# Kernel tuning notes

Measured on AMD Instinct MI355X. Metric: run time of the kernel, lower is better.

The kernel has to match this reference:

```python
import jax, jax.numpy as jnp
import numpy as np

N_NODES = 10000
N_PAIRS = 200000
NUM_FEATURES = 384
DEGREES = [1, 2, 3]
NHEADS = len(DEGREES)
F_HEAD = NUM_FEATURES // NHEADS  # 128
REPEATS = np.array([2 * d + 1 for d in DEGREES])  # [3,5,7]
SPH_DIM = int(REPEATS.sum())  # 15


def setup_inputs() -> dict:
    key = jax.random.key(0)
    ks = jax.random.split(key, 10)
    return {
        "chi": jax.random.normal(ks[0], (N_NODES, SPH_DIM), dtype=jnp.float32),
        "sph_ij": jax.random.normal(ks[1], (N_PAIRS, SPH_DIM), dtype=jnp.float32),
        "x": jax.random.normal(ks[2], (N_NODES, NUM_FEATURES), dtype=jnp.float32),
        "w_ij": jax.random.normal(ks[3], (N_PAIRS, NUM_FEATURES), dtype=jnp.float32),
        "idx_i": jax.random.randint(ks[4], (N_PAIRS,), 0, N_NODES),
        "phi_r_cut": jax.random.uniform(ks[5], (N_PAIRS, 1), dtype=jnp.float32),
        "phi_chi_cut": jax.random.uniform(ks[6], (N_PAIRS,), dtype=jnp.float32),
        "idx_j": jax.random.randint(ks[7], (N_PAIRS,), 0, N_NODES),
        # per-head linear weights (nn.Linear stores (out, in); y = x @ W.T)
        "Wq": jax.random.normal(ks[8], (NHEADS, F_HEAD, F_HEAD), dtype=jnp.float32) / np.sqrt(F_HEAD),
        "Wk": jax.random.normal(ks[9], (NHEADS, F_HEAD, F_HEAD), dtype=jnp.float32) / np.sqrt(F_HEAD),
    }


def reference(chi, sph_ij, x, w_ij, idx_i, phi_r_cut, phi_chi_cut, idx_j, Wq, Wk):
    n = x.shape[0]
    # split into heads: (n, H, Fh) / (E, H, Fh)
    x_h = x.reshape(n, NHEADS, F_HEAD)
    w_h = w_ij.reshape(-1, NHEADS, F_HEAD)
    # per-head linears (vmapped Linear, no bias): y = x @ W.T
    q = jnp.einsum("nhf,hgf->nhg", x_h, Wq)  # (n, H, Fh)
    k = jnp.einsum("nhf,hgf->nhg", x_h, Wk)  # (n, H, Fh)
    # gather + elementwise attention coefficients per head: (E, H)
    alpha = (q[idx_i] * w_h * k[idx_j]).sum(-1) / np.sqrt(F_HEAD).astype(np.float32)
    # combine radial and sphc cutoffs
    alpha = alpha * phi_r_cut + alpha * phi_chi_cut[:, None]  # (E, H)
    # repeat each head over its 2l+1 spherical components -> (E, SPH_DIM)
    alpha_rep = jnp.repeat(alpha, REPEATS, axis=-1, total_repeat_length=SPH_DIM)
    # scatter-add messages into center atoms -> (n, SPH_DIM)
    chi_ = jax.ops.segment_sum(alpha_rep * sph_ij, idx_i, num_segments=n)
    return chi_
```

## Files before the change

### kernel.cpp

```cpp
#include <hip/hip_runtime.h>
#include <hip/hip_bf16.h>

#define N_NODES 10000
#define N_PAIRS 200000
#define NFEAT 384
#define FH 128
#define SPH 15

typedef __bf16 bf16x8 __attribute__((ext_vector_type(8)));
typedef float f32x4 __attribute__((ext_vector_type(4)));

__global__ void cvt4_kernel(const float* __restrict__ in, unsigned short* __restrict__ out, int n4) {
    int t = blockIdx.x * blockDim.x + threadIdx.x;
    if (t >= n4) return;
    float4 v = ((const float4*)in)[t];
    __hip_bfloat16 b0 = __float2bfloat16(v.x);
    __hip_bfloat16 b1 = __float2bfloat16(v.y);
    __hip_bfloat16 b2 = __float2bfloat16(v.z);
    __hip_bfloat16 b3 = __float2bfloat16(v.w);
    ushort4 o;
    o.x = __builtin_bit_cast(unsigned short, b0);
    o.y = __builtin_bit_cast(unsigned short, b1);
    o.z = __builtin_bit_cast(unsigned short, b2);
    o.w = __builtin_bit_cast(unsigned short, b3);
    ((ushort4*)out)[t] = o;
}

__global__ void qk_gemm_kernel(const unsigned short* __restrict__ xb,
                               const unsigned short* __restrict__ Wqb,
                               const unsigned short* __restrict__ Wkb,
                               float* __restrict__ q, float* __restrict__ k) {
    const int head = blockIdx.y;
    const int node0 = blockIdx.x * 16;
    const int wave = threadIdx.x >> 6;
    const int lane = threadIdx.x & 63;
    const int mrow = lane & 15;
    const int quad = lane >> 4;
    const unsigned short* xrow = xb + (size_t)(node0 + mrow) * NFEAT + head * FH + quad * 8;
    for (int task = wave; task < 16; task += 4) {
        const int mat = task & 1;
        const int g0 = (task >> 1) * 16;
        const unsigned short* Wrow =
            (mat ? Wkb : Wqb) + (size_t)head * FH * FH + (size_t)(g0 + mrow) * FH + quad * 8;
        f32x4 acc = {0.f, 0.f, 0.f, 0.f};
#pragma unroll
        for (int k0 = 0; k0 < FH; k0 += 32) {
            bf16x8 a = *(const bf16x8*)(xrow + k0);
            bf16x8 b = *(const bf16x8*)(Wrow + k0);
            acc = __builtin_amdgcn_mfma_f32_16x16x32_bf16(a, b, acc, 0, 0, 0);
        }
        float* dst = mat ? k : q;
        const int g = g0 + (lane & 15);
#pragma unroll
        for (int r = 0; r < 4; ++r) {
            const int node = node0 + quad * 4 + r;
            dst[(size_t)node * NFEAT + head * FH + g] = acc[r];
        }
    }
}

__global__ void pair_kernel(const float* __restrict__ q, const float* __restrict__ kk,
                            const float* __restrict__ w_ij, const float* __restrict__ sph,
                            const int* __restrict__ idx_i, const int* __restrict__ idx_j,
                            const float* __restrict__ phi_r, const float* __restrict__ phi_chi,
                            float* __restrict__ out) {
    const int lane = threadIdx.x & 63;
    const int wid = blockIdx.x * (blockDim.x >> 6) + (threadIdx.x >> 6);
    const int nw = gridDim.x * (blockDim.x >> 6);
    for (int e = wid; e < N_PAIRS; e += nw) {
        const int i = idx_i[e];
        const int j = idx_j[e];
        const float* qr = q + (size_t)i * NFEAT;
        const float* kr = kk + (size_t)j * NFEAT;
        const float* wr = w_ij + (size_t)e * NFEAT;
        float dot[3];
#pragma unroll
        for (int h = 0; h < 3; ++h) {
            const int f = h * FH + 2 * lane;
            float2 q2 = *(const float2*)(qr + f);
            float2 w2 = *(const float2*)(wr + f);
            float2 k2 = *(const float2*)(kr + f);
            float p = q2.x * w2.x * k2.x + q2.y * w2.y * k2.y;
#pragma unroll
            for (int off = 32; off; off >>= 1) p += __shfl_xor(p, off, 64);
            dot[h] = p;
        }
        const float scale = (phi_r[e] + phi_chi[e]) * 0.088388347648318447f;
        if (lane < SPH) {
            const int h = (lane < 3) ? 0 : (lane < 8 ? 1 : 2);
            const float val = dot[h] * scale * sph[(size_t)e * SPH + lane];
            unsafeAtomicAdd(&out[(size_t)i * SPH + lane], val);
        }
    }
}

extern "C" void kernel_launch(void* const* d_in, const int* in_sizes, int n_in,
                              void* d_out, int out_size, void* d_ws, size_t ws_size,
                              hipStream_t stream) {
    const float* sph     = (const float*)d_in[1];
    const float* x       = (const float*)d_in[2];
    const float* w_ij    = (const float*)d_in[3];
    const int*   idx_i   = (const int*)d_in[4];
    const float* phi_r   = (const float*)d_in[5];
    const float* phi_chi = (const float*)d_in[6];
    const int*   idx_j   = (const int*)d_in[7];
    const float* Wq      = (const float*)d_in[8];
    const float* Wk      = (const float*)d_in[9];
    float* out = (float*)d_out;

    char* ws = (char*)d_ws;
    float* qws = (float*)ws;
    float* kws = (float*)(ws + 15360000);
    unsigned short* xb  = (unsigned short*)(ws + 30720000);
    unsigned short* Wqb = (unsigned short*)(ws + 38400000);
    unsigned short* Wkb = (unsigned short*)(ws + 38498304);

    hipMemsetAsync(d_out, 0, (size_t)out_size * sizeof(float), stream);

    cvt4_kernel<<<3750, 256, 0, stream>>>(x, xb, N_NODES * NFEAT / 4);
    cvt4_kernel<<<48, 256, 0, stream>>>(Wq, Wqb, 3 * FH * FH / 4);
    cvt4_kernel<<<48, 256, 0, stream>>>(Wk, Wkb, 3 * FH * FH / 4);

    qk_gemm_kernel<<<dim3(N_NODES / 16, 3), 256, 0, stream>>>(xb, Wqb, Wkb, qws, kws);

    pair_kernel<<<2048, 256, 0, stream>>>(qws, kws, w_ij, sph, idx_i, idx_j,
                                          phi_r, phi_chi, out);
}
```

Baseline: 507.7 us.

## Fuse bf16 conversion into QK GEMM and process four pairs per wave

```diff
diff --git a/kernel.cpp b/kernel.cpp
--- a/kernel.cpp
+++ b/kernel.cpp
@@ -10,25 +10,18 @@
 typedef __bf16 bf16x8 __attribute__((ext_vector_type(8)));
 typedef float f32x4 __attribute__((ext_vector_type(4)));
 
-__global__ void cvt4_kernel(const float* __restrict__ in, unsigned short* __restrict__ out, int n4) {
-    int t = blockIdx.x * blockDim.x + threadIdx.x;
-    if (t >= n4) return;
-    float4 v = ((const float4*)in)[t];
-    __hip_bfloat16 b0 = __float2bfloat16(v.x);
-    __hip_bfloat16 b1 = __float2bfloat16(v.y);
-    __hip_bfloat16 b2 = __float2bfloat16(v.z);
-    __hip_bfloat16 b3 = __float2bfloat16(v.w);
-    ushort4 o;
-    o.x = __builtin_bit_cast(unsigned short, b0);
-    o.y = __builtin_bit_cast(unsigned short, b1);
-    o.z = __builtin_bit_cast(unsigned short, b2);
-    o.w = __builtin_bit_cast(unsigned short, b3);
-    ((ushort4*)out)[t] = o;
+__device__ inline bf16x8 cvt8(const float* __restrict__ p) {
+    float4 lo = *(const float4*)p;
+    float4 hi = *(const float4*)(p + 4);
+    bf16x8 r;
+    r[0] = (__bf16)lo.x; r[1] = (__bf16)lo.y; r[2] = (__bf16)lo.z; r[3] = (__bf16)lo.w;
+    r[4] = (__bf16)hi.x; r[5] = (__bf16)hi.y; r[6] = (__bf16)hi.z; r[7] = (__bf16)hi.w;
+    return r;
 }
 
-__global__ void qk_gemm_kernel(const unsigned short* __restrict__ xb,
-                               const unsigned short* __restrict__ Wqb,
-                               const unsigned short* __restrict__ Wkb,
+__global__ void qk_gemm_kernel(const float* __restrict__ x,
+                               const float* __restrict__ Wq,
+                               const float* __restrict__ Wk,
                                float* __restrict__ q, float* __restrict__ k) {
     const int head = blockIdx.y;
     const int node0 = blockIdx.x * 16;
@@ -36,21 +29,24 @@
     const int lane = threadIdx.x & 63;
     const int mrow = lane & 15;
     const int quad = lane >> 4;
-    const unsigned short* xrow = xb + (size_t)(node0 + mrow) * NFEAT + head * FH + quad * 8;
+    const float* xrow = x + (size_t)(node0 + mrow) * NFEAT + head * FH + quad * 8;
+    bf16x8 afrag[4];
+#pragma unroll
+    for (int t = 0; t < 4; ++t) afrag[t] = cvt8(xrow + t * 32);
+
     for (int task = wave; task < 16; task += 4) {
         const int mat = task & 1;
         const int g0 = (task >> 1) * 16;
-        const unsigned short* Wrow =
-            (mat ? Wkb : Wqb) + (size_t)head * FH * FH + (size_t)(g0 + mrow) * FH + quad * 8;
+        const float* Wrow =
+            (mat ? Wk : Wq) + (size_t)head * FH * FH + (size_t)(g0 + mrow) * FH + quad * 8;
         f32x4 acc = {0.f, 0.f, 0.f, 0.f};
 #pragma unroll
-        for (int k0 = 0; k0 < FH; k0 += 32) {
-            bf16x8 a = *(const bf16x8*)(xrow + k0);
-            bf16x8 b = *(const bf16x8*)(Wrow + k0);
-            acc = __builtin_amdgcn_mfma_f32_16x16x32_bf16(a, b, acc, 0, 0, 0);
+        for (int t = 0; t < 4; ++t) {
+            bf16x8 b = cvt8(Wrow + t * 32);
+            acc = __builtin_amdgcn_mfma_f32_16x16x32_bf16(afrag[t], b, acc, 0, 0, 0);
         }
         float* dst = mat ? k : q;
-        const int g = g0 + (lane & 15);
+        const int g = g0 + mrow;
 #pragma unroll
         for (int r = 0; r < 4; ++r) {
             const int node = node0 + quad * 4 + r;
@@ -65,31 +61,46 @@
                             const float* __restrict__ phi_r, const float* __restrict__ phi_chi,
                             float* __restrict__ out) {
     const int lane = threadIdx.x & 63;
+    const int sub = lane & 15;
+    const int grp = lane >> 4;
     const int wid = blockIdx.x * (blockDim.x >> 6) + (threadIdx.x >> 6);
     const int nw = gridDim.x * (blockDim.x >> 6);
-    for (int e = wid; e < N_PAIRS; e += nw) {
-        const int i = idx_i[e];
-        const int j = idx_j[e];
-        const float* qr = q + (size_t)i * NFEAT;
-        const float* kr = kk + (size_t)j * NFEAT;
-        const float* wr = w_ij + (size_t)e * NFEAT;
-        float dot[3];
+    for (int base = wid * 4; base < N_PAIRS; base += nw * 4) {
+        const int e = base + grp;
+        if (e < N_PAIRS) {
+            const int i = idx_i[e];
+            const int j = idx_j[e];
+            const float* qr = q + (size_t)i * NFEAT;
+            const float* kr = kk + (size_t)j * NFEAT;
+            const float* wr = w_ij + (size_t)e * NFEAT;
+            float dot[3];
 #pragma unroll
-        for (int h = 0; h < 3; ++h) {
-            const int f = h * FH + 2 * lane;
-            float2 q2 = *(const float2*)(qr + f);
-            float2 w2 = *(const float2*)(wr + f);
-            float2 k2 = *(const float2*)(kr + f);
-            float p = q2.x * w2.x * k2.x + q2.y * w2.y * k2.y;
+            for (int h = 0; h < 3; ++h) {
+                const int f = h * FH + sub * 8;
+                float4 qa = *(const float4*)(qr + f);
+                float4 qb = *(const float4*)(qr + f + 4);
+                float4 wa = *(const float4*)(wr + f);
+                float4 wb = *(const float4*)(wr + f + 4);
+                float4 ka = *(const float4*)(kr + f);
+                float4 kb = *(const float4*)(kr + f + 4);
+                float p = qa.x * wa.x * ka.x;
+                p = fmaf(qa.y * wa.y, ka.y, p);
+                p = fmaf(qa.z * wa.z, ka.z, p);
+                p = fmaf(qa.w * wa.w, ka.w, p);
+                p = fmaf(qb.x * wb.x, kb.x, p);
+                p = fmaf(qb.y * wb.y, kb.y, p);
+                p = fmaf(qb.z * wb.z, kb.z, p);
+                p = fmaf(qb.w * wb.w, kb.w, p);
 #pragma unroll
-            for (int off = 32; off; off >>= 1) p += __shfl_xor(p, off, 64);
-            dot[h] = p;
-        }
-        const float scale = (phi_r[e] + phi_chi[e]) * 0.088388347648318447f;
-        if (lane < SPH) {
-            const int h = (lane < 3) ? 0 : (lane < 8 ? 1 : 2);
-            const float val = dot[h] * scale * sph[(size_t)e * SPH + lane];
-            unsafeAtomicAdd(&out[(size_t)i * SPH + lane], val);
+                for (int off = 8; off; off >>= 1) p += __shfl_xor(p, off, 16);
+                dot[h] = p;
+            }
+            const float scale = (phi_r[e] + phi_chi[e]) * 0.088388347648318447f;
+            if (sub < SPH) {
+                const int h = (sub < 3) ? 0 : (sub < 8 ? 1 : 2);
+                const float val = dot[h] * scale * sph[(size_t)e * SPH + sub];
+                unsafeAtomicAdd(&out[(size_t)i * SPH + sub], val);
+            }
         }
     }
 }
@@ -111,17 +122,10 @@
     char* ws = (char*)d_ws;
     float* qws = (float*)ws;
     float* kws = (float*)(ws + 15360000);
-    unsigned short* xb  = (unsigned short*)(ws + 30720000);
-    unsigned short* Wqb = (unsigned short*)(ws + 38400000);
-    unsigned short* Wkb = (unsigned short*)(ws + 38498304);
 
     hipMemsetAsync(d_out, 0, (size_t)out_size * sizeof(float), stream);
 
-    cvt4_kernel<<<3750, 256, 0, stream>>>(x, xb, N_NODES * NFEAT / 4);
-    cvt4_kernel<<<48, 256, 0, stream>>>(Wq, Wqb, 3 * FH * FH / 4);
-    cvt4_kernel<<<48, 256, 0, stream>>>(Wk, Wkb, 3 * FH * FH / 4);
-
-    qk_gemm_kernel<<<dim3(N_NODES / 16, 3), 256, 0, stream>>>(xb, Wqb, Wkb, qws, kws);
+    qk_gemm_kernel<<<dim3(N_NODES / 16, 3), 256, 0, stream>>>(x, Wq, Wk, qws, kws);
 
     pair_kernel<<<2048, 256, 0, stream>>>(qws, kws, w_ij, sph, idx_i, idx_j,
                                           phi_r, phi_chi, out);
```

After: 502.8 us. No clear change (-1.0%).
